# Performance work log

Measured on AMD Instinct MI355X. Metric: run time of the kernel, lower is better.

The kernel has to match this reference:

```python
import jax, jax.numpy as jnp
import numpy as np

S, C, H, D = 4096, 2048, 16, 128  # seq, channels, heads, head_dim
EPS = 1.1920929e-07  # torch F.rms_norm default eps = finfo(float32).eps


def setup_inputs() -> dict:
    key = jax.random.key(0)
    ks = jax.random.split(key, 12)
    w = 0.02
    return {
        "x": jax.random.normal(ks[0], (S, C), dtype=jnp.float32),
        "rope": jax.random.normal(ks[1], (S, 1, D // 2, 2, 2), dtype=jnp.float32),
        "Wq": jax.random.normal(ks[2], (C, C), dtype=jnp.float32) * w,
        "bq": jnp.zeros((C,), dtype=jnp.float32),
        "Wk": jax.random.normal(ks[3], (C, C), dtype=jnp.float32) * w,
        "bk": jnp.zeros((C,), dtype=jnp.float32),
        "Wv": jax.random.normal(ks[4], (C, C), dtype=jnp.float32) * w,
        "bv": jnp.zeros((C,), dtype=jnp.float32),
        "qn_w": jnp.ones((D,), dtype=jnp.float32),
        "kn_w": jnp.ones((D,), dtype=jnp.float32),
        "Wo": jax.random.normal(ks[5], (C, C), dtype=jnp.float32) * w,
        "bo": jnp.zeros((C,), dtype=jnp.float32),
    }


def _rms_norm(x, weight):
    # RMSNorm over last dim, as F.rms_norm
    inv = jax.lax.rsqrt(jnp.mean(x * x, axis=-1, keepdims=True) + EPS)
    return x * inv * weight


def _apply_rotary(x, rope):
    # x: [S, H, D]; rope: [S, 1, D//2, 2, 2]
    s, h, d = x.shape
    x_ = x.reshape(s, h, d // 2, 1, 2)
    out = (rope * x_).sum(axis=-1)  # [S, H, D//2, 2]
    return out.reshape(s, h, d)


def reference(x, rope, Wq, bq, Wk, bk, Wv, bv, qn_w, kn_w, Wo, bo):
    # QKV projections -> [S, H, D]
    q = (x @ Wq.T + bq).reshape(S, H, D)
    k = (x @ Wk.T + bk).reshape(S, H, D)
    v = (x @ Wv.T + bv).reshape(S, H, D)
    # RMSNorm on q/k per head_dim
    q = _rms_norm(q, qn_w)
    k = _rms_norm(k, kn_w)
    # Custom rotary (table-driven 2x2 rotation)
    q = _apply_rotary(q, rope)
    k = _apply_rotary(k, rope)
    # Dense scaled dot-product attention over seq, per head
    scale = 1.0 / jnp.sqrt(jnp.asarray(D, dtype=q.dtype))
    scores = jnp.einsum("shd,thd->hst", q, k) * scale  # [H, S, S]
    probs = jax.nn.softmax(scores, axis=-1)
    out = jnp.einsum("hst,thd->shd", probs, v).reshape(S, C)
    return out @ Wo.T + bo
```

## Files before the change

kernel.cpp:

```cpp
#include <hip/hip_runtime.h>

#define S 4096
#define C 2048
#define H 16
#define D 128
#define EPS 1.1920929e-07f
#define QSCALE (0.08838834764831845f * 1.4426950408889634f)
#define BN 64
#define NT (S / BN)
#define GBM 256
#define GBN 128
#define GBK 64
#define NKT (C / GBK)
#define GBUF (GBM * GBK + GBN * GBK)

typedef __attribute__((ext_vector_type(8))) short short8;
typedef __attribute__((ext_vector_type(4))) float f32x4;
typedef __attribute__((ext_vector_type(4))) unsigned int uint4v;

#if __has_builtin(__builtin_amdgcn_exp2f)
#define EXP2F __builtin_amdgcn_exp2f
#else
#define EXP2F exp2f
#endif

__device__ __forceinline__ unsigned short f2bf(float f) {
  unsigned int u = __builtin_bit_cast(unsigned int, f);
  u += 0x7fff + ((u >> 16) & 1);
  return (unsigned short)(u >> 16);
}
__device__ __forceinline__ float bf2f(unsigned short v) {
  unsigned int u = ((unsigned int)v) << 16;
  return __builtin_bit_cast(float, u);
}
__device__ __forceinline__ unsigned int pkbf(float a, float b) {
  return (unsigned int)f2bf(a) | ((unsigned int)f2bf(b) << 16);
}
__device__ __forceinline__ unsigned int pkbf_trunc(float a, float b) {
  return __builtin_amdgcn_perm(__builtin_bit_cast(unsigned int, b),
                               __builtin_bit_cast(unsigned int, a), 0x07060302);
}
__device__ __forceinline__ void gld16(const unsigned short* g, unsigned short* l) {
  __builtin_amdgcn_global_load_lds(
      (const __attribute__((address_space(1))) unsigned int*)g,
      (__attribute__((address_space(3))) unsigned int*)l, 16, 0, 0);
}
__device__ __forceinline__ short8 mk_a(unsigned int a, unsigned int b,
                                       unsigned int c, unsigned int d) {
  uint4v u;
  u[0] = a; u[1] = b; u[2] = c; u[3] = d;
  return __builtin_bit_cast(short8, u);
}

__global__ void cvt_kernel(const float* __restrict__ src,
                           unsigned short* __restrict__ dst, int n) {
  int i = (blockIdx.x * 256 + threadIdx.x) * 4;
  if (i >= n) return;
  float4 v = *(const float4*)(src + i);
  ushort4 o;
  o.x = f2bf(v.x); o.y = f2bf(v.y); o.z = f2bf(v.z); o.w = f2bf(v.w);
  *(ushort4*)(dst + i) = o;
}
__global__ void cvtw_kernel(const float* __restrict__ w0, const float* __restrict__ w1,
                            const float* __restrict__ w2, const float* __restrict__ w3,
                            unsigned short* __restrict__ dst) {
  const float* srcs[4] = {w0, w1, w2, w3};
  const float* src = srcs[blockIdx.y];
  int i = (blockIdx.x * 256 + threadIdx.x) * 4;
  float4 v = *(const float4*)(src + i);
  ushort4 o;
  o.x = f2bf(v.x); o.y = f2bf(v.y); o.z = f2bf(v.z); o.w = f2bf(v.w);
  *(ushort4*)(dst + (size_t)blockIdx.y * C * C + i) = o;
}
__global__ void bias_concat(const float* __restrict__ bq, const float* __restrict__ bk,
                            const float* __restrict__ bv, float* __restrict__ dst) {
  int i = blockIdx.x * 256 + threadIdx.x;
  const float* s = (i < C) ? bq : ((i < 2 * C) ? bk : bv);
  dst[i] = s[i & (C - 1)];
}

__global__ __launch_bounds__(512, 2) void gemm_bt(const unsigned short* __restrict__ A,
                                                  const unsigned short* __restrict__ B,
                                                  const float* __restrict__ bias,
                                                  float* __restrict__ outf,
                                                  unsigned short* __restrict__ qh,
                                                  unsigned short* __restrict__ kh,
                                                  unsigned short* __restrict__ vt,
                                                  int N, int mode) {
  __shared__ __align__(16) unsigned short L[3 * GBUF];
  const int t = threadIdx.x, w = t >> 6, lane = t & 63;
  const int lq = lane & 15, quad = lane >> 4;
  const int wm = w >> 1, wn = w & 1;

  const int nwg = gridDim.x * gridDim.y;
  int id = blockIdx.x * gridDim.y + blockIdx.y;
  int nid = (id & 7) * (nwg >> 3) + (id >> 3);
  const int bx = nid / (int)gridDim.y, by = nid % (int)gridDim.y;
  const int m0 = by * GBM, n0 = bx * GBN;

  f32x4 acc[4][4] = {};
  float biasv[4];
#pragma unroll
  for (int nt = 0; nt < 4; nt++) biasv[nt] = bias[n0 + wn * 64 + nt * 16 + lq];

  const int srow = lane >> 3, sg = lane & 7;
  auto stage = [&](int tt, int b) {
    unsigned short* Ab = L + b * GBUF;
    unsigned short* Bb = Ab + GBM * GBK;
    const int k0 = tt * GBK;
#pragma unroll
    for (int p = 0; p < 4; p++) {
      int row = p * 64 + w * 8 + srow;
      int c = sg ^ (row & 7);
      gld16(A + (size_t)(m0 + row) * C + k0 + c * 8, Ab + (p * 64 + w * 8) * GBK);
    }
#pragma unroll
    for (int p = 0; p < 2; p++) {
      int row = p * 64 + w * 8 + srow;
      int c = sg ^ (row & 7);
      gld16(B + (size_t)(n0 + row) * C + k0 + c * 8, Bb + (p * 64 + w * 8) * GBK);
    }
  };

  stage(0, 0);
  stage(1, 1);

  int cb = 0;
  for (int tt = 0; tt < NKT; ++tt) {
    if (tt < NKT - 1)
      asm volatile("s_waitcnt vmcnt(6)" ::: "memory");
    else
      asm volatile("s_waitcnt vmcnt(0)" ::: "memory");
    __builtin_amdgcn_s_barrier();
    asm volatile("" ::: "memory");
    if (tt + 2 < NKT) {
      int sb = cb + 2; if (sb >= 3) sb -= 3;
      stage(tt + 2, sb);
    }
    unsigned short* Ab = L + cb * GBUF;
    unsigned short* Bb = Ab + GBM * GBK;
    short8 af[4][2], bf[4][2];
#pragma unroll
    for (int mt = 0; mt < 4; mt++) {
      int row = wm * 64 + mt * 16 + lq;
#pragma unroll
      for (int ks = 0; ks < 2; ks++)
        af[mt][ks] = *(const short8*)&Ab[row * GBK + (((ks * 4 + quad) ^ (row & 7)) * 8)];
    }
#pragma unroll
    for (int nt = 0; nt < 4; nt++) {
      int row = wn * 64 + nt * 16 + lq;
#pragma unroll
      for (int ks = 0; ks < 2; ks++)
        bf[nt][ks] = *(const short8*)&Bb[row * GBK + (((ks * 4 + quad) ^ (row & 7)) * 8)];
    }
    __builtin_amdgcn_s_setprio(1);
#pragma unroll
    for (int ks = 0; ks < 2; ks++)
#pragma unroll
      for (int mt = 0; mt < 4; mt++)
#pragma unroll
        for (int nt = 0; nt < 4; nt++)
          acc[mt][nt] = __builtin_amdgcn_mfma_f32_16x16x32_bf16(af[mt][ks], bf[nt][ks], acc[mt][nt], 0, 0, 0);
    __builtin_amdgcn_s_setprio(0);
    cb = (cb == 2) ? 0 : cb + 1;
  }

  if (mode == 0) {
#pragma unroll
    for (int mt = 0; mt < 4; mt++)
#pragma unroll
      for (int nt = 0; nt < 4; nt++) {
        int n = n0 + wn * 64 + nt * 16 + lq;
#pragma unroll
        for (int r = 0; r < 4; r++) {
          int m = m0 + wm * 64 + mt * 16 + quad * 4 + r;
          outf[(size_t)m * N + n] = acc[mt][nt][r] + biasv[nt];
        }
      }
    return;
  }

  const int gh = bx;
  __syncthreads();
  if (gh < 32) {
    unsigned short* U = L;
#pragma unroll
    for (int mt = 0; mt < 4; mt++)
#pragma unroll
      for (int nt = 0; nt < 4; nt++) {
        int dloc = wn * 64 + nt * 16 + lq;
#pragma unroll
        for (int r = 0; r < 4; r++)
          U[(wm * 64 + mt * 16 + quad * 4 + r) * 136 + dloc] = f2bf(acc[mt][nt][r] + biasv[nt]);
      }
    __syncthreads();
    unsigned short* dst = ((gh < 16) ? qh : kh) + (size_t)(gh & 15) * S * D;
    const int rr = t >> 4, ck = t & 15;
#pragma unroll
    for (int p = 0; p < 8; p++) {
      int m = p * 32 + rr;
      uint4 vv = *(const uint4*)&U[m * 136 + ck * 8];
      *(uint4*)(dst + (size_t)(m0 + m) * D + ck * 8) = vv;
    }
  } else {
    unsigned short* U = L;
#pragma unroll
    for (int mt = 0; mt < 4; mt++)
#pragma unroll
      for (int nt = 0; nt < 4; nt++) {
        int dloc = wn * 64 + nt * 16 + lq;
        int mlocP = wm * 64 + (mt >> 1) * 32 + quad * 8 + (mt & 1) * 4;
        *(unsigned int*)&U[dloc * 264 + mlocP] =
            pkbf(acc[mt][nt][0] + biasv[nt], acc[mt][nt][1] + biasv[nt]);
        *(unsigned int*)&U[dloc * 264 + mlocP + 2] =
            pkbf(acc[mt][nt][2] + biasv[nt], acc[mt][nt][3] + biasv[nt]);
      }
    __syncthreads();
    unsigned short* dst = vt + (size_t)(gh - 32) * D * S;
    const int rr = t >> 5, ck = t & 31;
#pragma unroll
    for (int p = 0; p < 8; p++) {
      int d = p * 16 + rr;
      uint4 vv = *(const uint4*)&U[d * 264 + ck * 8];
      *(uint4*)(dst + (size_t)d * S + m0 + ck * 8) = vv;
    }
  }
}

__global__ __launch_bounds__(256) void rmsrope_kernel(unsigned short* __restrict__ qh,
                                                      unsigned short* __restrict__ kh,
                                                      const float* __restrict__ qn_w,
                                                      const float* __restrict__ kn_w,
                                                      const float* __restrict__ rope) {
  const int which = blockIdx.y;
  unsigned short* io = which ? kh : qh;
  const float* wgt = which ? kn_w : qn_w;
  const float scale = which ? 1.0f : QSCALE;
  int wid = (blockIdx.x * 256 + threadIdx.x) >> 6;
  int lane = threadIdx.x & 63;
  int s = wid & (S - 1);
  unsigned short* row = io + (size_t)wid * D;
  unsigned int pr = *(unsigned int*)(row + lane * 2);
  float a = bf2f((unsigned short)(pr & 0xffff));
  float b = bf2f((unsigned short)(pr >> 16));
  float ss = a * a + b * b;
  for (int m = 1; m < 64; m <<= 1) ss += __shfl_xor(ss, m);
  float inv = rsqrtf(ss * (1.0f / 128.0f) + EPS) * scale;
  float2 wv = *(const float2*)(wgt + lane * 2);
  float an = a * inv * wv.x, bn = b * inv * wv.y;
  float4 r = *(const float4*)(rope + (size_t)s * 256 + lane * 4);
  *(unsigned int*)(row + lane * 2) = pkbf(r.x * an + r.y * bn, r.z * an + r.w * bn);
}

__global__ __launch_bounds__(256, 2) void flash_kernel(const unsigned short* __restrict__ qh,
                                                       const unsigned short* __restrict__ kh,
                                                       const unsigned short* __restrict__ vt,
                                                       unsigned short* __restrict__ ao) {
  __shared__ __align__(16) unsigned short Klds[2 * BN * D];
  __shared__ __align__(16) unsigned short Vlds[2 * D * BN];
  const int d_id = blockIdx.y * gridDim.x + blockIdx.x;
  const int xcd = d_id & 7, p_id = d_id >> 3;
  const int h = 2 * xcd + (p_id >> 5);
  const int i0 = (p_id & 31) * 128;
  const int t = threadIdx.x, w = t >> 6, lane = t & 63;
  const int lq = lane & 15, quad = lane >> 4;

  const unsigned short* Qbase = qh + ((size_t)h * S + i0 + w * 32 + lq) * D;
  short8 qfrag[2][4];
#pragma unroll
  for (int qi = 0; qi < 2; qi++)
#pragma unroll
    for (int kt = 0; kt < 4; kt++)
      qfrag[qi][kt] = *(const short8*)(Qbase + (size_t)qi * 16 * D + kt * 32 + quad * 8);

  f32x4 oacc[2][8] = {};
  f32x4 dacc[2] = {};
  const unsigned short* Kbase = kh + (size_t)h * S * D;
  const unsigned short* Vbase = vt + (size_t)h * D * S;

  const int k_r = lane >> 4, k_g = lane & 15;
  const int v_r = lane >> 3, v_g = lane & 7;

  uint4v onesu;
  onesu[0] = 0x3F803F80u; onesu[1] = 0x3F803F80u; onesu[2] = 0x3F803F80u; onesu[3] = 0x3F803F80u;
  const short8 ones = __builtin_bit_cast(short8, onesu);

#pragma unroll
  for (int p = 0; p < 4; p++) {
    int kr = w * 16 + p * 4 + k_r;
    gld16(Kbase + (size_t)kr * D + (k_g ^ (kr & 7)) * 8, &Klds[(w * 16 + p * 4) * D]);
  }
#pragma unroll
  for (int p = 0; p < 4; p++) {
    int vr = w * 32 + p * 8 + v_r;
    gld16(Vbase + (size_t)vr * S + (v_g ^ (vr & 7)) * 8, &Vlds[(w * 32 + p * 8) * BN]);
  }

  for (int tt = 0; tt < NT; ++tt) {
    const int cur = tt & 1;
    unsigned short* Kc = Klds + cur * (BN * D);
    unsigned short* Vc = Vlds + cur * (D * BN);
    __syncthreads();
    if (tt + 1 < NT) {
      const int j1 = (tt + 1) * BN;
      unsigned short* Kn = Klds + (cur ^ 1) * (BN * D);
      unsigned short* Vn = Vlds + (cur ^ 1) * (D * BN);
#pragma unroll
      for (int p = 0; p < 4; p++) {
        int kr = w * 16 + p * 4 + k_r;
        gld16(Kbase + (size_t)(j1 + kr) * D + (k_g ^ (kr & 7)) * 8, &Kn[(w * 16 + p * 4) * D]);
      }
#pragma unroll
      for (int p = 0; p < 4; p++) {
        int vr = w * 32 + p * 8 + v_r;
        gld16(Vbase + (size_t)vr * S + j1 + (v_g ^ (vr & 7)) * 8, &Vn[(w * 32 + p * 8) * BN]);
      }
    }

    f32x4 sacc[2][4] = {};
    __builtin_amdgcn_s_setprio(1);
#pragma unroll
    for (int kt = 0; kt < 4; kt++)
#pragma unroll
      for (int nt = 0; nt < 4; nt++) {
        int row = nt * 16 + lq;
        short8 af = *(const short8*)&Kc[row * D + (((kt * 4 + quad) ^ (row & 7)) * 8)];
        sacc[0][nt] = __builtin_amdgcn_mfma_f32_16x16x32_bf16(af, qfrag[0][kt], sacc[0][nt], 0, 0, 0);
        sacc[1][nt] = __builtin_amdgcn_mfma_f32_16x16x32_bf16(af, qfrag[1][kt], sacc[1][nt], 0, 0, 0);
      }
    __builtin_amdgcn_s_setprio(0);

    unsigned int pd[2][4][2];
#pragma unroll
    for (int qi = 0; qi < 2; qi++)
#pragma unroll
      for (int nt = 0; nt < 4; nt++) {
        float e0 = EXP2F(sacc[qi][nt][0]);
        float e1 = EXP2F(sacc[qi][nt][1]);
        float e2 = EXP2F(sacc[qi][nt][2]);
        float e3 = EXP2F(sacc[qi][nt][3]);
        pd[qi][nt][0] = pkbf_trunc(e0, e1);
        pd[qi][nt][1] = pkbf_trunc(e2, e3);
      }

    __builtin_amdgcn_s_setprio(1);
#pragma unroll
    for (int kk = 0; kk < 2; kk++) {
      short8 a0 = mk_a(pd[0][2 * kk][0], pd[0][2 * kk][1], pd[0][2 * kk + 1][0], pd[0][2 * kk + 1][1]);
      short8 a1 = mk_a(pd[1][2 * kk][0], pd[1][2 * kk][1], pd[1][2 * kk + 1][0], pd[1][2 * kk + 1][1]);
      dacc[0] = __builtin_amdgcn_mfma_f32_16x16x32_bf16(a0, ones, dacc[0], 0, 0, 0);
      dacc[1] = __builtin_amdgcn_mfma_f32_16x16x32_bf16(a1, ones, dacc[1], 0, 0, 0);
#pragma unroll
      for (int dt = 0; dt < 8; dt++) {
        int row = dt * 16 + lq;
        short8 bf = *(const short8*)&Vc[row * BN + (((kk * 4 + quad) ^ (row & 7)) * 8)];
        oacc[0][dt] = __builtin_amdgcn_mfma_f32_16x16x32_bf16(a0, bf, oacc[0][dt], 0, 0, 0);
        oacc[1][dt] = __builtin_amdgcn_mfma_f32_16x16x32_bf16(a1, bf, oacc[1][dt], 0, 0, 0);
      }
    }
    __builtin_amdgcn_s_setprio(0);
  }

  float il[2][4];
#pragma unroll
  for (int qi = 0; qi < 2; qi++)
#pragma unroll
    for (int r = 0; r < 4; r++) il[qi][r] = 1.0f / dacc[qi][r];
#pragma unroll
  for (int qi = 0; qi < 2; qi++)
#pragma unroll
    for (int dt = 0; dt < 8; dt++)
#pragma unroll
      for (int r = 0; r < 4; r++)
        ao[(size_t)(i0 + w * 32 + qi * 16 + quad * 4 + r) * C + h * 128 + dt * 16 + lq] =
            f2bf(oacc[qi][dt][r] * il[qi][r]);
}

extern "C" void kernel_launch(void* const* d_in, const int* in_sizes, int n_in,
                              void* d_out, int out_size, void* d_ws, size_t ws_size,
                              hipStream_t stream) {
  const float* x    = (const float*)d_in[0];
  const float* rope = (const float*)d_in[1];
  const float* Wq   = (const float*)d_in[2];
  const float* bq   = (const float*)d_in[3];
  const float* Wk   = (const float*)d_in[4];
  const float* bk   = (const float*)d_in[5];
  const float* Wv   = (const float*)d_in[6];
  const float* bv   = (const float*)d_in[7];
  const float* qn_w = (const float*)d_in[8];
  const float* kn_w = (const float*)d_in[9];
  const float* Wo   = (const float*)d_in[10];
  const float* bo   = (const float*)d_in[11];
  float* out = (float*)d_out;

  unsigned short* xb  = (unsigned short*)d_ws;
  unsigned short* wqb = xb + (size_t)S * C;
  unsigned short* wob = wqb + (size_t)3 * C * C;
  unsigned short* qh  = wqb + (size_t)4 * C * C;
  unsigned short* kh  = qh + (size_t)S * C;
  unsigned short* vt  = kh + (size_t)S * C;
  unsigned short* ao  = vt + (size_t)S * C;
  float* bqkv = (float*)(ao + (size_t)S * C);

  cvt_kernel<<<S * C / 1024, 256, 0, stream>>>(x, xb, S * C);
  cvtw_kernel<<<dim3(C * C / 1024, 4), 256, 0, stream>>>(Wq, Wk, Wv, Wo, wqb);
  bias_concat<<<3 * C / 256, 256, 0, stream>>>(bq, bk, bv, bqkv);

  gemm_bt<<<dim3(3 * C / GBN, S / GBM), 512, 0, stream>>>(
      xb, wqb, bqkv, nullptr, qh, kh, vt, 3 * C, 1);

  rmsrope_kernel<<<dim3((H * S) / 4, 2), 256, 0, stream>>>(qh, kh, qn_w, kn_w, rope);

  flash_kernel<<<dim3(S / 128, H), 256, 0, stream>>>(qh, kh, vt, ao);

  gemm_bt<<<dim3(C / GBN, S / GBM), 512, 0, stream>>>(
      ao, wob, bo, out, nullptr, nullptr, nullptr, C, 0);
}
```

Before: 441.2 us.

## Software-pipeline flash attention so QK of next tile overlaps softmax-PV

The flash attention inner loop is restructured into a two-stage software pipeline. The QK^T MFMAs for tile t+1 are issued alongside the exp/softmax and PV work for tile t, using two score accumulator sets and separately staged K and V buffers. The aim is to hide exp latency and LDS waits behind matrix work. Holding twice the score accumulators raises register pressure, so launch bounds drop from 2 to 1 blocks per CU, which risks lower occupancy and less latency hiding between blocks.

```diff
diff --git a/kernel.cpp b/kernel.cpp
--- a/kernel.cpp
+++ b/kernel.cpp
@@ -8,6 +8,8 @@
 #define QSCALE (0.08838834764831845f * 1.4426950408889634f)
 #define BN 64
 #define NT (S / BN)
+#define KBUF (BN * D)
+#define VBUF (D * BN)
 #define GBM 256
 #define GBN 128
 #define GBK 64
@@ -253,12 +255,12 @@
   *(unsigned int*)(row + lane * 2) = pkbf(r.x * an + r.y * bn, r.z * an + r.w * bn);
 }
 
-__global__ __launch_bounds__(256, 2) void flash_kernel(const unsigned short* __restrict__ qh,
+__global__ __launch_bounds__(256, 1) void flash_kernel(const unsigned short* __restrict__ qh,
                                                        const unsigned short* __restrict__ kh,
                                                        const unsigned short* __restrict__ vt,
                                                        unsigned short* __restrict__ ao) {
-  __shared__ __align__(16) unsigned short Klds[2 * BN * D];
-  __shared__ __align__(16) unsigned short Vlds[2 * D * BN];
+  __shared__ __align__(16) unsigned short Klds[2 * KBUF];
+  __shared__ __align__(16) unsigned short Vlds[2 * VBUF];
   const int d_id = blockIdx.y * gridDim.x + blockIdx.x;
   const int xcd = d_id & 7, p_id = d_id >> 3;
   const int h = 2 * xcd + (p_id >> 5);
@@ -286,39 +288,25 @@
   onesu[0] = 0x3F803F80u; onesu[1] = 0x3F803F80u; onesu[2] = 0x3F803F80u; onesu[3] = 0x3F803F80u;
   const short8 ones = __builtin_bit_cast(short8, onesu);
 
-#pragma unroll
-  for (int p = 0; p < 4; p++) {
-    int kr = w * 16 + p * 4 + k_r;
-    gld16(Kbase + (size_t)kr * D + (k_g ^ (kr & 7)) * 8, &Klds[(w * 16 + p * 4) * D]);
-  }
-#pragma unroll
-  for (int p = 0; p < 4; p++) {
-    int vr = w * 32 + p * 8 + v_r;
-    gld16(Vbase + (size_t)vr * S + (v_g ^ (vr & 7)) * 8, &Vlds[(w * 32 + p * 8) * BN]);
-  }
-
-  for (int tt = 0; tt < NT; ++tt) {
-    const int cur = tt & 1;
-    unsigned short* Kc = Klds + cur * (BN * D);
-    unsigned short* Vc = Vlds + cur * (D * BN);
-    __syncthreads();
-    if (tt + 1 < NT) {
-      const int j1 = (tt + 1) * BN;
-      unsigned short* Kn = Klds + (cur ^ 1) * (BN * D);
-      unsigned short* Vn = Vlds + (cur ^ 1) * (D * BN);
-#pragma unroll
-      for (int p = 0; p < 4; p++) {
-        int kr = w * 16 + p * 4 + k_r;
-        gld16(Kbase + (size_t)(j1 + kr) * D + (k_g ^ (kr & 7)) * 8, &Kn[(w * 16 + p * 4) * D]);
-      }
-#pragma unroll
-      for (int p = 0; p < 4; p++) {
-        int vr = w * 32 + p * 8 + v_r;
-        gld16(Vbase + (size_t)vr * S + j1 + (v_g ^ (vr & 7)) * 8, &Vn[(w * 32 + p * 8) * BN]);
-      }
-    }
-
-    f32x4 sacc[2][4] = {};
+  auto stageK = [&](int jt, unsigned short* Kb) {
+#pragma unroll
+    for (int p = 0; p < 4; p++) {
+      int kr = w * 16 + p * 4 + k_r;
+      gld16(Kbase + ((size_t)jt * BN + kr) * D + (k_g ^ (kr & 7)) * 8, &Kb[(w * 16 + p * 4) * D]);
+    }
+  };
+  auto stageV = [&](int jt, unsigned short* Vb) {
+#pragma unroll
+    for (int p = 0; p < 4; p++) {
+      int vr = w * 32 + p * 8 + v_r;
+      gld16(Vbase + (size_t)vr * S + jt * BN + (v_g ^ (vr & 7)) * 8, &Vb[(w * 32 + p * 8) * BN]);
+    }
+  };
+  auto qk_into = [&](const unsigned short* Kc, f32x4 (&sn)[2][4]) {
+#pragma unroll
+    for (int qi = 0; qi < 2; qi++)
+#pragma unroll
+      for (int nt = 0; nt < 4; nt++) sn[qi][nt] = (f32x4){0.f, 0.f, 0.f, 0.f};
     __builtin_amdgcn_s_setprio(1);
 #pragma unroll
     for (int kt = 0; kt < 4; kt++)
@@ -326,24 +314,24 @@
       for (int nt = 0; nt < 4; nt++) {
         int row = nt * 16 + lq;
         short8 af = *(const short8*)&Kc[row * D + (((kt * 4 + quad) ^ (row & 7)) * 8)];
-        sacc[0][nt] = __builtin_amdgcn_mfma_f32_16x16x32_bf16(af, qfrag[0][kt], sacc[0][nt], 0, 0, 0);
-        sacc[1][nt] = __builtin_amdgcn_mfma_f32_16x16x32_bf16(af, qfrag[1][kt], sacc[1][nt], 0, 0, 0);
+        sn[0][nt] = __builtin_amdgcn_mfma_f32_16x16x32_bf16(af, qfrag[0][kt], sn[0][nt], 0, 0, 0);
+        sn[1][nt] = __builtin_amdgcn_mfma_f32_16x16x32_bf16(af, qfrag[1][kt], sn[1][nt], 0, 0, 0);
       }
     __builtin_amdgcn_s_setprio(0);
-
+  };
+  auto sm_pv = [&](f32x4 (&sc)[2][4], const unsigned short* Vc) {
     unsigned int pd[2][4][2];
 #pragma unroll
     for (int qi = 0; qi < 2; qi++)
 #pragma unroll
       for (int nt = 0; nt < 4; nt++) {
-        float e0 = EXP2F(sacc[qi][nt][0]);
-        float e1 = EXP2F(sacc[qi][nt][1]);
-        float e2 = EXP2F(sacc[qi][nt][2]);
-        float e3 = EXP2F(sacc[qi][nt][3]);
+        float e0 = EXP2F(sc[qi][nt][0]);
+        float e1 = EXP2F(sc[qi][nt][1]);
+        float e2 = EXP2F(sc[qi][nt][2]);
+        float e3 = EXP2F(sc[qi][nt][3]);
         pd[qi][nt][0] = pkbf_trunc(e0, e1);
         pd[qi][nt][1] = pkbf_trunc(e2, e3);
       }
-
     __builtin_amdgcn_s_setprio(1);
 #pragma unroll
     for (int kk = 0; kk < 2; kk++) {
@@ -360,6 +348,26 @@
       }
     }
     __builtin_amdgcn_s_setprio(0);
+  };
+
+  stageK(0, Klds);
+  stageK(1, Klds + KBUF);
+  stageV(0, Vlds);
+  __syncthreads();
+  f32x4 saccA[2][4], saccB[2][4];
+  qk_into(Klds, saccA);
+
+  for (int tt = 0; tt < NT; tt += 2) {
+    __syncthreads();
+    if (tt + 2 < NT) stageK(tt + 2, Klds);
+    stageV(tt + 1, Vlds + VBUF);
+    qk_into(Klds + KBUF, saccB);
+    sm_pv(saccA, Vlds);
+    __syncthreads();
+    if (tt + 3 < NT) stageK(tt + 3, Klds + KBUF);
+    if (tt + 2 < NT) stageV(tt + 2, Vlds);
+    if (tt + 2 < NT) qk_into(Klds, saccA);
+    sm_pv(saccB, Vlds + VBUF);
   }
 
   float il[2][4];
```

Result: slower. 519.7 us (+17.8%).
